# Optimization experiments

Measured on AMD Instinct MI355X. Metric: run time of the kernel, lower is better.

## Reference

```python
import jax, jax.numpy as jnp
import numpy as np

N_EMBD = 384
N_HEAD = 6
HEAD_SIZE = N_EMBD // N_HEAD  # 64
B, T, S = 128, 256, 256
EPS = 1e-5


def setup_inputs() -> dict:
    key = jax.random.key(0)
    ks = jax.random.split(key, 20)
    w = lambda k, shape: (jax.random.normal(k, shape, dtype=jnp.float32) * 0.02)
    inp = {
        'x': jax.random.normal(ks[0], (B, T, N_EMBD), dtype=jnp.float32),
        'encoder_output': jax.random.normal(ks[1], (B, S, N_EMBD), dtype=jnp.float32),
        # masked self-attention heads (stacked over heads): [H, C, D]
        'wq1': w(ks[2], (N_HEAD, N_EMBD, HEAD_SIZE)),
        'wk1': w(ks[3], (N_HEAD, N_EMBD, HEAD_SIZE)),
        'wv1': w(ks[4], (N_HEAD, N_EMBD, HEAD_SIZE)),
        'proj1_w': w(ks[5], (N_EMBD, N_EMBD)),
        'proj1_b': jnp.zeros((N_EMBD,), jnp.float32),
        # cross-attention heads
        'wq2': w(ks[6], (N_HEAD, N_EMBD, HEAD_SIZE)),
        'wk2': w(ks[7], (N_HEAD, N_EMBD, HEAD_SIZE)),
        'wv2': w(ks[8], (N_HEAD, N_EMBD, HEAD_SIZE)),
        'proj2_w': w(ks[9], (N_EMBD, N_EMBD)),
        'proj2_b': jnp.zeros((N_EMBD,), jnp.float32),
        # feed-forward
        'ffn_w1': w(ks[10], (N_EMBD, 4 * N_EMBD)),
        'ffn_b1': jnp.zeros((4 * N_EMBD,), jnp.float32),
        'ffn_w2': w(ks[11], (4 * N_EMBD, N_EMBD)),
        'ffn_b2': jnp.zeros((N_EMBD,), jnp.float32),
        # layernorms
        'ln1_g': jnp.ones((N_EMBD,), jnp.float32), 'ln1_b': jnp.zeros((N_EMBD,), jnp.float32),
        'ln2_g': jnp.ones((N_EMBD,), jnp.float32), 'ln2_b': jnp.zeros((N_EMBD,), jnp.float32),
        'ln3_g': jnp.ones((N_EMBD,), jnp.float32), 'ln3_b': jnp.zeros((N_EMBD,), jnp.float32),
    }
    return inp


def _layernorm(x, g, b):
    mu = jnp.mean(x, axis=-1, keepdims=True)
    var = jnp.mean(jnp.square(x - mu), axis=-1, keepdims=True)
    return (x - mu) * jax.lax.rsqrt(var + EPS) * g + b


def _mha(xq, xkv, wq, wk, wv, proj_w, proj_b, causal):
    # NOTE: source scales by C**-0.5 with C = n_embd (not head_size)
    scale = jnp.asarray(N_EMBD, xq.dtype) ** -0.5
    q = jnp.einsum('btc,hcd->bhtd', xq, wq)
    k = jnp.einsum('bsc,hcd->bhsd', xkv, wk)
    v = jnp.einsum('bsc,hcd->bhsd', xkv, wv)
    wei = jnp.einsum('bhtd,bhsd->bhts', q, k) * scale
    if causal:
        Tq, Tk = xq.shape[1], xkv.shape[1]
        mask = jnp.tril(jnp.ones((Tq, Tk), dtype=bool))
        wei = jnp.where(mask, wei, jnp.asarray(-jnp.inf, wei.dtype))
    p = jax.nn.softmax(wei, axis=-1)  # dropout omitted (eval mode)
    o = jnp.einsum('bhts,bhsd->bhtd', p, v)
    Bq, H, Tq, D = o.shape
    o = o.transpose(0, 2, 1, 3).reshape(Bq, Tq, H * D)  # concat heads
    return o @ proj_w + proj_b


def reference(x, encoder_output,
              wq1, wk1, wv1, proj1_w, proj1_b,
              wq2, wk2, wv2, proj2_w, proj2_b,
              ffn_w1, ffn_b1, ffn_w2, ffn_b2,
              ln1_g, ln1_b, ln2_g, ln2_b, ln3_g, ln3_b):
    # x = x + masked self-attn(ln1(x))
    x = x + _mha(_layernorm(x, ln1_g, ln1_b), _layernorm(x, ln1_g, ln1_b),
                 wq1, wk1, wv1, proj1_w, proj1_b, causal=True)
    # x = x + cross-attn(ln2(x), encoder_output)  (no mask)
    x = x + _mha(_layernorm(x, ln2_g, ln2_b), encoder_output,
                 wq2, wk2, wv2, proj2_w, proj2_b, causal=False)
    # x = x + ffwd(ln3(x))
    h = _layernorm(x, ln3_g, ln3_b)
    x = x + (jax.nn.relu(h @ ffn_w1 + ffn_b1) @ ffn_w2 + ffn_b2)
    return x
```

## Files before the change

### kernel.cpp

```cpp
#include <hip/hip_runtime.h>
#include <hip/hip_bf16.h>

#define BB 128
#define TT 256
#define CC 384
#define HH 6
#define DD 64
#define NTOK 32768

typedef __attribute__((ext_vector_type(8))) short short8;
typedef __attribute__((ext_vector_type(4))) float f32x4;

__device__ __forceinline__ unsigned short f2bf(float f) {
  union { float f; unsigned int u; } v; v.f = f;
  unsigned int r = v.u + 0x7fff + ((v.u >> 16) & 1);
  return (unsigned short)(r >> 16);
}

__device__ __forceinline__ void glds16(const void* g, void* l) {
  __builtin_amdgcn_global_load_lds((const __attribute__((address_space(1))) void*)g,
                                   (__attribute__((address_space(3))) void*)l, 16, 0, 0);
}

__device__ __forceinline__ void vm_drain() {
  asm volatile("s_waitcnt vmcnt(0)" ::: "memory");
  __builtin_amdgcn_sched_barrier(0);
}

__global__ __launch_bounds__(256) void pack_t_k(
    const float* __restrict__ wq1, const float* __restrict__ wk1, const float* __restrict__ wv1,
    const float* __restrict__ wq2, const float* __restrict__ wk2, const float* __restrict__ wv2,
    const float* __restrict__ proj1_w, const float* __restrict__ proj2_w,
    const float* __restrict__ ffn_w1, const float* __restrict__ ffn_w2,
    unsigned short* __restrict__ W) {
  __shared__ unsigned short tile[64 * 72];
  const int id = blockIdx.x;
  const int tid = threadIdx.x;
  const float* src;
  unsigned short* dst;
  int ldIn, ldOut, i0, j0;
  if (id < 216) {
    int w = id / 36, rem = id - w * 36;
    int h = rem / 6, tr = rem - h * 6;
    const float* bases[6] = {wq1, wk1, wv1, wq2, wk2, wv2};
    const int dstOff[6] = {0, 147456, 294912, 442368, 589824, 737280};
    src = bases[w] + h * 24576;
    dst = W + dstOff[w] + h * 24576;
    ldIn = 64; ldOut = 384; i0 = tr * 64; j0 = 0;
  } else if (id < 288) {
    int t = id - 216;
    int which = t / 36; t -= which * 36;
    int tr = t / 6, tc = t - tr * 6;
    src = which ? proj2_w : proj1_w;
    dst = W + (which ? 1032192 : 884736);
    ldIn = 384; ldOut = 384; i0 = tr * 64; j0 = tc * 64;
  } else if (id < 432) {
    int t = id - 288;
    int tr = t / 24, tc = t - tr * 24;
    src = ffn_w1; dst = W + 1179648;
    ldIn = 1536; ldOut = 384; i0 = tr * 64; j0 = tc * 64;
  } else {
    int t = id - 432;
    int tr = t / 6, tc = t - tr * 6;
    src = ffn_w2; dst = W + 1769472;
    ldIn = 384; ldOut = 1536; i0 = tr * 64; j0 = tc * 64;
  }
#pragma unroll
  for (int p = 0; p < 4; ++p) {
    int chunk = p * 256 + tid;
    int r = chunk >> 4, c4 = chunk & 15;
    float4 f = *(const float4*)&src[(size_t)(i0 + r) * ldIn + j0 + c4 * 4];
    tile[(c4 * 4 + 0) * 72 + r] = f2bf(f.x);
    tile[(c4 * 4 + 1) * 72 + r] = f2bf(f.y);
    tile[(c4 * 4 + 2) * 72 + r] = f2bf(f.z);
    tile[(c4 * 4 + 3) * 72 + r] = f2bf(f.w);
  }
  __syncthreads();
#pragma unroll
  for (int p = 0; p < 2; ++p) {
    int chunk = p * 256 + tid;
    int j = chunk >> 3, i8 = chunk & 7;
    *(uint4*)&dst[(size_t)(j0 + j) * ldOut + i0 + i8 * 8] = *(const uint4*)&tile[j * 72 + i8 * 8];
  }
}

__global__ __launch_bounds__(256) void ln_k(const float* __restrict__ x,
                                            unsigned short* __restrict__ out,
                                            const float* __restrict__ gamma,
                                            const float* __restrict__ beta) {
  int row = blockIdx.x * 4 + (threadIdx.x >> 6);
  int lane = threadIdx.x & 63;
  const float2* xr = (const float2*)(x + (size_t)row * CC);
  float2 v[3];
  float s = 0.f;
#pragma unroll
  for (int j = 0; j < 3; ++j) { v[j] = xr[j * 64 + lane]; s += v[j].x + v[j].y; }
#pragma unroll
  for (int m = 1; m < 64; m <<= 1) s += __shfl_xor(s, m);
  float mu = s * (1.0f / CC);
  float vs = 0.f;
#pragma unroll
  for (int j = 0; j < 3; ++j) {
    float dx = v[j].x - mu, dy = v[j].y - mu;
    vs += dx * dx + dy * dy;
  }
#pragma unroll
  for (int m = 1; m < 64; m <<= 1) vs += __shfl_xor(vs, m);
  float rs = rsqrtf(vs * (1.0f / CC) + 1e-5f);
  unsigned int* orow = (unsigned int*)(out + (size_t)row * CC);
#pragma unroll
  for (int j = 0; j < 3; ++j) {
    int cidx = j * 64 + lane;
    float2 gmm = ((const float2*)gamma)[cidx];
    float2 bt = ((const float2*)beta)[cidx];
    unsigned int lo = f2bf((v[j].x - mu) * rs * gmm.x + bt.x);
    unsigned int hi = f2bf((v[j].y - mu) * rs * gmm.y + bt.y);
    orow[cidx] = lo | (hi << 16);
  }
}

template <int EPI, bool AF32, int BM>
__global__ __launch_bounds__(256) void gemm_k(const void* __restrict__ Ap, int lda,
                                              const unsigned short* __restrict__ Bt, int ldb,
                                              void* __restrict__ Cp, int ldc,
                                              const float* __restrict__ bias,
                                              const float* __restrict__ res, int ldres,
                                              int K, int nx) {
  constexpr int MI = BM / 32;
  constexpr int APASS = BM * 8 / 256;
  constexpr int SMEMN = (EPI == 2) ? (BM * 256) : (BM * 64 + 8192);
  __shared__ unsigned short smem[SMEMN];
  unsigned short* sA = smem;
  unsigned short* sB = smem + BM * 64;
  const int tid = threadIdx.x;
  const int chunkg = gridDim.x >> 3;
  const int wg = blockIdx.x;
  const int lg = (wg & 7) * chunkg + (wg >> 3);
  const int bx = lg % nx, by = lg / nx;
  const int m0 = by * BM;
  const int n0 = bx * 128;
  const int wid = tid >> 6, lane = tid & 63;
  const int wr = wid >> 1, wc = wid & 1;
  const int g = lane >> 4, c = lane & 15;

  f32x4 acc[MI][4] = {};
  float biasr[4];
  if (EPI >= 1) {
#pragma unroll
    for (int ni = 0; ni < 4; ++ni) biasr[ni] = bias[n0 + wc * 64 + ni * 16 + c];
  }

  const int nt = K >> 6;
  for (int t = 0; t < nt; ++t) {
    const int k0 = t * 64;
    if constexpr (!AF32) {
#pragma unroll
      for (int p = 0; p < APASS; ++p) {
        int chunk = p * 256 + tid;
        int row = chunk >> 3, grp = chunk & 7;
        const unsigned short* Ab = (const unsigned short*)Ap;
        glds16(&Ab[(size_t)(m0 + row) * lda + k0 + ((grp ^ (row & 7)) << 3)], &sA[chunk * 8]);
      }
    } else {
#pragma unroll
      for (int p = 0; p < APASS; ++p) {
        int chunk = p * 256 + tid;
        int row = chunk >> 3, grp = chunk & 7;
        int dst = row * 64 + ((grp ^ (row & 7)) << 3);
        const float* Af = (const float*)Ap + (size_t)(m0 + row) * lda + k0 + grp * 8;
        float4 f0 = *(const float4*)Af;
        float4 f1 = *(const float4*)(Af + 4);
        union { unsigned short h[8]; uint4 u; } t2;
        t2.h[0] = f2bf(f0.x); t2.h[1] = f2bf(f0.y); t2.h[2] = f2bf(f0.z); t2.h[3] = f2bf(f0.w);
        t2.h[4] = f2bf(f1.x); t2.h[5] = f2bf(f1.y); t2.h[6] = f2bf(f1.z); t2.h[7] = f2bf(f1.w);
        *(uint4*)&sA[dst] = t2.u;
      }
    }
#pragma unroll
    for (int p = 0; p < 4; ++p) {
      int chunk = p * 256 + tid;
      int row = chunk >> 3, grp = chunk & 7;
      glds16(&Bt[(size_t)(n0 + row) * ldb + k0 + ((grp ^ (row & 7)) << 3)], &sB[chunk * 8]);
    }
    vm_drain();
    __syncthreads();
#pragma unroll
    for (int kk = 0; kk < 2; ++kk) {
      short8 a[MI], b[4];
#pragma unroll
      for (int mi = 0; mi < MI; ++mi) {
        int r = wr * (BM / 2) + mi * 16 + c;
        a[mi] = *(const short8*)&sA[r * 64 + (((kk * 4 + g) ^ (r & 7)) << 3)];
      }
#pragma unroll
      for (int ni = 0; ni < 4; ++ni) {
        int rb = wc * 64 + ni * 16 + c;
        b[ni] = *(const short8*)&sB[rb * 64 + (((kk * 4 + g) ^ (rb & 7)) << 3)];
      }
#pragma unroll
      for (int mi = 0; mi < MI; ++mi)
#pragma unroll
        for (int ni = 0; ni < 4; ++ni)
          acc[mi][ni] = __builtin_amdgcn_mfma_f32_16x16x32_bf16(a[mi], b[ni], acc[mi][ni], 0, 0, 0);
    }
    __syncthreads();
  }

  if (EPI <= 1) {
#pragma unroll
    for (int mi = 0; mi < MI; ++mi)
#pragma unroll
      for (int ni = 0; ni < 4; ++ni)
#pragma unroll
        for (int i = 0; i < 4; ++i) {
          int row = wr * (BM / 2) + mi * 16 + g * 4 + i;
          int col = wc * 64 + ni * 16 + c;
          float v = acc[mi][ni][i];
          if (EPI == 1) v = fmaxf(v + biasr[ni], 0.f);
          int gsw = (col >> 3) ^ ((row >> 2) & 7);
          smem[row * 128 + gsw * 8 + (col & 7)] = f2bf(v);
        }
    __syncthreads();
#pragma unroll
    for (int it = 0; it < BM / 16; ++it) {
      int chunk = it * 256 + tid;
      int row = chunk >> 4, c16 = chunk & 15;
      int gsw = c16 ^ ((row >> 2) & 7);
      *(uint4*)&((unsigned short*)Cp)[(size_t)(m0 + row) * ldc + n0 + c16 * 8] =
          *(const uint4*)&smem[row * 128 + gsw * 8];
    }
  } else {
    float* smf = (float*)smem;
#pragma unroll
    for (int mi = 0; mi < MI; ++mi)
#pragma unroll
      for (int ni = 0; ni < 4; ++ni)
#pragma unroll
        for (int i = 0; i < 4; ++i) {
          int row = wr * (BM / 2) + mi * 16 + g * 4 + i;
          int col = wc * 64 + ni * 16 + c;
          int gg = col >> 2;
          int sg = gg ^ (row & 7);
          smf[row * 128 + sg * 4 + (col & 3)] = acc[mi][ni][i] + biasr[ni];
        }
    __syncthreads();
#pragma unroll
    for (int it = 0; it < BM / 8; ++it) {
      int chunk = it * 256 + tid;
      int row = chunk >> 5, gg = chunk & 31;
      int sg = gg ^ (row & 7);
      float4 v = *(const float4*)&smf[row * 128 + sg * 4];
      float4 r = *(const float4*)&res[(size_t)(m0 + row) * ldres + n0 + gg * 4];
      float4 o;
      o.x = v.x + r.x; o.y = v.y + r.y; o.z = v.z + r.z; o.w = v.w + r.w;
      *(float4*)&((float*)Cp)[(size_t)(m0 + row) * ldc + n0 + gg * 4] = o;
    }
  }
}

__global__ __launch_bounds__(512, 2) void gemm_ln_k(
    const unsigned short* __restrict__ Ab, const unsigned short* __restrict__ Bt,
    const float* __restrict__ bias, const float* __restrict__ res,
    float* __restrict__ xc, const float* __restrict__ gamma,
    const float* __restrict__ beta, unsigned short* __restrict__ xn) {
  __shared__ unsigned short smem[28672];
  __shared__ float part[64][8];
  unsigned short* sA = smem;
  unsigned short* sB = smem + 4096;
  const int tid = threadIdx.x;
  const int chunkg = gridDim.x >> 3;
  const int wg = blockIdx.x;
  const int lg = (wg & 7) * chunkg + (wg >> 3);
  const int m0 = lg * 64;
  const int wid = tid >> 6, lane = tid & 63;
  const int wr = wid >> 2, wcg = wid & 3;
  const int g = lane >> 4, c = lane & 15;

  f32x4 acc[2][6] = {};
  float biasr[6], gam[6], bet[6];
#pragma unroll
  for (int ni = 0; ni < 6; ++ni) {
    int col = wcg * 96 + ni * 16 + c;
    biasr[ni] = bias[col]; gam[ni] = gamma[col]; bet[ni] = beta[col];
  }

  for (int t = 0; t < 6; ++t) {
    const int k0 = t * 64;
    {
      int chunk = tid;
      int row = chunk >> 3, grp = chunk & 7;
      glds16(&Ab[(size_t)(m0 + row) * 384 + k0 + ((grp ^ (row & 7)) << 3)], &sA[chunk * 8]);
    }
#pragma unroll
    for (int p = 0; p < 6; ++p) {
      int chunk = p * 512 + tid;
      int row = chunk >> 3, grp = chunk & 7;
      glds16(&Bt[(size_t)row * 384 + k0 + ((grp ^ (row & 7)) << 3)], &sB[chunk * 8]);
    }
    vm_drain();
    __syncthreads();
#pragma unroll
    for (int kk = 0; kk < 2; ++kk) {
      short8 a[2], b[6];
#pragma unroll
      for (int mi = 0; mi < 2; ++mi) {
        int r = wr * 32 + mi * 16 + c;
        a[mi] = *(const short8*)&sA[r * 64 + (((kk * 4 + g) ^ (r & 7)) << 3)];
      }
#pragma unroll
      for (int ni = 0; ni < 6; ++ni) {
        int rb = wcg * 96 + ni * 16 + c;
        b[ni] = *(const short8*)&sB[rb * 64 + (((kk * 4 + g) ^ (rb & 7)) << 3)];
      }
#pragma unroll
      for (int mi = 0; mi < 2; ++mi)
#pragma unroll
        for (int ni = 0; ni < 6; ++ni)
          acc[mi][ni] = __builtin_amdgcn_mfma_f32_16x16x32_bf16(a[mi], b[ni], acc[mi][ni], 0, 0, 0);
    }
    __syncthreads();
  }

#pragma unroll
  for (int mi = 0; mi < 2; ++mi)
#pragma unroll
    for (int i = 0; i < 4; ++i) {
      int row = m0 + wr * 32 + mi * 16 + g * 4 + i;
#pragma unroll
      for (int ni = 0; ni < 6; ++ni)
        acc[mi][ni][i] += biasr[ni] + res[(size_t)row * 384 + wcg * 96 + ni * 16 + c];
    }

#pragma unroll
  for (int mi = 0; mi < 2; ++mi)
#pragma unroll
    for (int i = 0; i < 4; ++i) {
      float s = 0.f, q = 0.f;
#pragma unroll
      for (int ni = 0; ni < 6; ++ni) { float v = acc[mi][ni][i]; s += v; q += v * v; }
#pragma unroll
      for (int m = 1; m < 16; m <<= 1) { s += __shfl_xor(s, m); q += __shfl_xor(q, m); }
      if (c == 0) {
        int lr = wr * 32 + mi * 16 + g * 4 + i;
        part[lr][wcg] = s;
        part[lr][4 + wcg] = q;
      }
    }
  __syncthreads();
  float mu[2][4], rs[2][4];
#pragma unroll
  for (int mi = 0; mi < 2; ++mi)
#pragma unroll
    for (int i = 0; i < 4; ++i) {
      int lr = wr * 32 + mi * 16 + g * 4 + i;
      float s = part[lr][0] + part[lr][1] + part[lr][2] + part[lr][3];
      float q = part[lr][4] + part[lr][5] + part[lr][6] + part[lr][7];
      float m_ = s * (1.0f / 384.f);
      mu[mi][i] = m_;
      rs[mi][i] = rsqrtf(q * (1.0f / 384.f) - m_ * m_ + 1e-5f);
    }

  float* bf = (float*)smem;
#pragma unroll
  for (int h = 0; h < 2; ++h) {
    __syncthreads();
    if (wr == h) {
#pragma unroll
      for (int mi = 0; mi < 2; ++mi)
#pragma unroll
        for (int ni = 0; ni < 6; ++ni)
#pragma unroll
          for (int i = 0; i < 4; ++i) {
            int lr = mi * 16 + g * 4 + i;
            bf[lr * 388 + wcg * 96 + ni * 16 + c] = acc[mi][ni][i];
          }
    }
    __syncthreads();
#pragma unroll
    for (int p = 0; p < 6; ++p) {
      int chunk = p * 512 + tid;
      int row = chunk / 96, gg = chunk % 96;
      float4 v = *(const float4*)&bf[row * 388 + gg * 4];
      *(float4*)&xc[(size_t)(m0 + h * 32 + row) * 384 + gg * 4] = v;
    }
  }

  __syncthreads();
#pragma unroll
  for (int mi = 0; mi < 2; ++mi)
#pragma unroll
    for (int ni = 0; ni < 6; ++ni)
#pragma unroll
      for (int i = 0; i < 4; ++i) {
        int lr = wr * 32 + mi * 16 + g * 4 + i;
        smem[lr * 392 + wcg * 96 + ni * 16 + c] =
            f2bf((acc[mi][ni][i] - mu[mi][i]) * rs[mi][i] * gam[ni] + bet[ni]);
      }
  __syncthreads();
#pragma unroll
  for (int p = 0; p < 6; ++p) {
    int chunk = p * 512 + tid;
    int row = chunk / 48, c8 = chunk % 48;
    *(uint4*)&xn[(size_t)(m0 + row) * 384 + c8 * 8] = *(const uint4*)&smem[row * 392 + c8 * 8];
  }
}

__device__ __forceinline__ int vt_off(int d, int sgrp) {
  return d * 256 + ((((sgrp + (d >> 3)) & 31) ^ (d & 7)) << 3);
}

template <bool CAUSAL>
__global__ __launch_bounds__(512, 2) void attn_k(const unsigned short* __restrict__ QKV,
                                                 unsigned short* __restrict__ O) {
  __shared__ unsigned short Ks[256 * 64];
  __shared__ unsigned short Vt[64 * 256];
  __shared__ unsigned short Ps[8][16 * 40];
  const int bh = blockIdx.x >> 1;
  const int half = blockIdx.x & 1;
  const int b = bh / HH, hh = bh - b * HH;
  const int tid = threadIdx.x, wid = tid >> 6, lane = tid & 63;
  const int g = lane >> 4, c = lane & 15;
  const unsigned short* base = QKV + (size_t)b * TT * 1152;

#pragma unroll
  for (int t = 0; t < 4; ++t) {
    int chunk = t * 512 + tid;
    int s = chunk >> 3, grp = chunk & 7;
    *(uint4*)&Ks[s * 64 + ((grp ^ (s & 7)) << 3)] =
        *(const uint4*)&base[(size_t)s * 1152 + 384 + hh * 64 + grp * 8];
    union { unsigned short h[8]; uint4 u; } tv;
    tv.u = *(const uint4*)&base[(size_t)s * 1152 + 768 + hh * 64 + grp * 8];
#pragma unroll
    for (int j = 0; j < 8; ++j) Vt[vt_off(grp * 8 + j, s >> 3) + (s & 7)] = tv.h[j];
  }
  __syncthreads();

  const float scale = 0.05103103630798287f;
  unsigned short* Pw = &Ps[wid][0];
  const int qr0 = half * 128 + wid * 16;

  short8 aq[2];
#pragma unroll
  for (int kk = 0; kk < 2; ++kk)
    aq[kk] = *(const short8*)&QKV[(size_t)(b * TT + qr0 + c) * 1152 + hh * 64 + kk * 32 + g * 8];

  f32x4 sacc[16] = {};
#pragma unroll
  for (int sj = 0; sj < 16; ++sj) {
    if (!CAUSAL || sj * 16 <= qr0) {
      int rk = sj * 16 + c;
      f32x4 z = sacc[sj];
      z = __builtin_amdgcn_mfma_f32_16x16x32_bf16(
          aq[0], *(const short8*)&Ks[rk * 64 + ((g ^ (rk & 7)) << 3)], z, 0, 0, 0);
      z = __builtin_amdgcn_mfma_f32_16x16x32_bf16(
          aq[1], *(const short8*)&Ks[rk * 64 + (((4 + g) ^ (rk & 7)) << 3)], z, 0, 0, 0);
      sacc[sj] = z;
    }
  }

  float inv[4];
#pragma unroll
  for (int i = 0; i < 4; ++i) {
    const int qr = qr0 + g * 4 + i;
    float mx = -1e30f;
#pragma unroll
    for (int sj = 0; sj < 16; ++sj) {
      if (!CAUSAL || sj * 16 <= qr0) {
        int s = sj * 16 + c;
        float v = sacc[sj][i] * scale;
        if (CAUSAL && s > qr) v = -1e30f;
        sacc[sj][i] = v;
        mx = fmaxf(mx, v);
      }
    }
#pragma unroll
    for (int m = 1; m < 16; m <<= 1) mx = fmaxf(mx, __shfl_xor(mx, m));
    float sum = 0.f;
#pragma unroll
    for (int sj = 0; sj < 16; ++sj) {
      if (!CAUSAL || sj * 16 <= qr0) {
        float p = __expf(sacc[sj][i] - mx);
        sacc[sj][i] = p;
        sum += p;
      }
    }
#pragma unroll
    for (int m = 1; m < 16; m <<= 1) sum += __shfl_xor(sum, m);
    inv[i] = 1.0f / sum;
  }

  f32x4 oacc[4] = {};
#pragma unroll
  for (int sk = 0; sk < 8; ++sk) {
    if (!CAUSAL || sk * 32 <= qr0) {
#pragma unroll
      for (int half_sj = 0; half_sj < 2; ++half_sj) {
        int sj = sk * 2 + half_sj;
#pragma unroll
        for (int i = 0; i < 4; ++i)
          Pw[(g * 4 + i) * 40 + half_sj * 16 + c] = f2bf(sacc[sj][i]);
      }
      short8 ap = *(const short8*)&Pw[c * 40 + g * 8];
#pragma unroll
      for (int dj = 0; dj < 4; ++dj) {
        short8 bv = *(const short8*)&Vt[vt_off(dj * 16 + c, sk * 4 + g)];
        oacc[dj] = __builtin_amdgcn_mfma_f32_16x16x32_bf16(ap, bv, oacc[dj], 0, 0, 0);
      }
    }
  }

  __syncthreads();
#pragma unroll
  for (int dj = 0; dj < 4; ++dj)
#pragma unroll
    for (int i = 0; i < 4; ++i) {
      int lr = wid * 16 + g * 4 + i;
      int col = dj * 16 + c;
      int gsw = (col >> 3) ^ ((lr >> 2) & 7);
      Ks[lr * 64 + gsw * 8 + (col & 7)] = f2bf(oacc[dj][i] * inv[i]);
    }
  __syncthreads();
#pragma unroll
  for (int it = 0; it < 2; ++it) {
    int chunk = it * 512 + tid;
    int row = chunk >> 3, c8 = chunk & 7;
    int gsw = c8 ^ ((row >> 2) & 7);
    *(uint4*)&O[(size_t)(b * TT + half * 128 + row) * CC + hh * 64 + c8 * 8] =
        *(const uint4*)&Ks[row * 64 + gsw * 8];
  }
}

extern "C" void kernel_launch(void* const* d_in, const int* in_sizes, int n_in,
                              void* d_out, int out_size, void* d_ws, size_t ws_size,
                              hipStream_t stream) {
  const float* x = (const float*)d_in[0];
  const float* enc = (const float*)d_in[1];
  const float* wq1 = (const float*)d_in[2];
  const float* wk1 = (const float*)d_in[3];
  const float* wv1 = (const float*)d_in[4];
  const float* proj1_w = (const float*)d_in[5];
  const float* proj1_b = (const float*)d_in[6];
  const float* wq2 = (const float*)d_in[7];
  const float* wk2 = (const float*)d_in[8];
  const float* wv2 = (const float*)d_in[9];
  const float* proj2_w = (const float*)d_in[10];
  const float* proj2_b = (const float*)d_in[11];
  const float* ffn_w1 = (const float*)d_in[12];
  const float* ffn_b1 = (const float*)d_in[13];
  const float* ffn_w2 = (const float*)d_in[14];
  const float* ffn_b2 = (const float*)d_in[15];
  const float* ln1_g = (const float*)d_in[16];
  const float* ln1_b = (const float*)d_in[17];
  const float* ln2_g = (const float*)d_in[18];
  const float* ln2_b = (const float*)d_in[19];
  const float* ln3_g = (const float*)d_in[20];
  const float* ln3_b = (const float*)d_in[21];
  float* out = (float*)d_out;

  char* ws = (char*)d_ws;
  const size_t OFF_A = 0;
  const size_t OFF_X = 50331648;
  const size_t OFF_Q = 75497472;
  const size_t OFF_O = 150994944;
  const size_t OFF_W = 176160768;

  float* xc = (float*)(ws + OFF_A);
  unsigned short* xn = (unsigned short*)(ws + OFF_X);
  unsigned short* qkv = (unsigned short*)(ws + OFF_Q);
  unsigned short* h1 = (unsigned short*)(ws + OFF_Q);
  unsigned short* obuf = (unsigned short*)(ws + OFF_O);
  unsigned short* W = (unsigned short*)(ws + OFF_W);

  unsigned short* Wqkv1t = W + 0;
  unsigned short* Wq2t = W + 442368;
  unsigned short* Wkv2t = W + 589824;
  unsigned short* proj1t = W + 884736;
  unsigned short* proj2t = W + 1032192;
  unsigned short* W1t = W + 1179648;
  unsigned short* W2t = W + 1769472;

  pack_t_k<<<576, 256, 0, stream>>>(wq1, wk1, wv1, wq2, wk2, wv2,
                                    proj1_w, proj2_w, ffn_w1, ffn_w2, W);

  dim3 blk(256);
  ln_k<<<8192, blk, 0, stream>>>(x, xn, ln1_g, ln1_b);
  gemm_k<0, false, 128><<<2304, blk, 0, stream>>>(xn, 384, Wqkv1t, 384, qkv, 1152,
                                                  nullptr, nullptr, 0, 384, 9);
  attn_k<true><<<1536, 512, 0, stream>>>(qkv, obuf);
  gemm_ln_k<<<512, 512, 0, stream>>>(obuf, proj1t, proj1_b, x, xc, ln2_g, ln2_b, xn);
  gemm_k<0, false, 128><<<768, blk, 0, stream>>>(xn, 384, Wq2t, 384, qkv, 1152,
                                                 nullptr, nullptr, 0, 384, 3);
  gemm_k<0, true, 128><<<1536, blk, 0, stream>>>(enc, 384, Wkv2t, 384, qkv + 384, 1152,
                                                 nullptr, nullptr, 0, 384, 6);
  attn_k<false><<<1536, 512, 0, stream>>>(qkv, obuf);
  gemm_ln_k<<<512, 512, 0, stream>>>(obuf, proj2t, proj2_b, xc, xc, ln3_g, ln3_b, xn);
  gemm_k<1, false, 128><<<3072, blk, 0, stream>>>(xn, 384, W1t, 384, h1, 1536,
                                                  ffn_b1, nullptr, 0, 384, 12);
  gemm_k<2, false, 64><<<1536, blk, 0, stream>>>(h1, 1536, W2t, 1536, out, 384,
                                                 ffn_b2, xc, 384, 1536, 3);
}
```

Before: 399.2 us.

## Process all query rows per attention block and enlarge FFN2 GEMM tile

Each attention block now covers all 256 query rows of a batch-head instead of half. Every warp handles two 16-row query blocks, so K and V are staged into LDS once per head rather than twice, and the grid halves. The FFN2 GEMM moves from 64-row to 128-row tiles. Its fp32 residual epilogue is staged through shared memory in two 64-row halves so the LDS footprint stays fixed. The trade-off is fewer blocks, which means more wave-quantization tail and, in the causal case, more uneven work across warps.

```diff
diff --git a/kernel.cpp b/kernel.cpp
--- a/kernel.cpp
+++ b/kernel.cpp
@@ -128,7 +128,7 @@
                                               int K, int nx) {
   constexpr int MI = BM / 32;
   constexpr int APASS = BM * 8 / 256;
-  constexpr int SMEMN = (EPI == 2) ? (BM * 256) : (BM * 64 + 8192);
+  constexpr int SMEMN = BM * 64 + 8192;
   __shared__ unsigned short smem[SMEMN];
   unsigned short* sA = smem;
   unsigned short* sB = smem + BM * 64;
@@ -230,30 +230,38 @@
           *(const uint4*)&smem[row * 128 + gsw * 8];
     }
   } else {
+    constexpr int NH = BM / 64;
     float* smf = (float*)smem;
 #pragma unroll
-    for (int mi = 0; mi < MI; ++mi)
-#pragma unroll
-      for (int ni = 0; ni < 4; ++ni)
-#pragma unroll
-        for (int i = 0; i < 4; ++i) {
-          int row = wr * (BM / 2) + mi * 16 + g * 4 + i;
-          int col = wc * 64 + ni * 16 + c;
-          int gg = col >> 2;
-          int sg = gg ^ (row & 7);
-          smf[row * 128 + sg * 4 + (col & 3)] = acc[mi][ni][i] + biasr[ni];
-        }
-    __syncthreads();
-#pragma unroll
-    for (int it = 0; it < BM / 8; ++it) {
-      int chunk = it * 256 + tid;
-      int row = chunk >> 5, gg = chunk & 31;
-      int sg = gg ^ (row & 7);
-      float4 v = *(const float4*)&smf[row * 128 + sg * 4];
-      float4 r = *(const float4*)&res[(size_t)(m0 + row) * ldres + n0 + gg * 4];
-      float4 o;
-      o.x = v.x + r.x; o.y = v.y + r.y; o.z = v.z + r.z; o.w = v.w + r.w;
-      *(float4*)&((float*)Cp)[(size_t)(m0 + row) * ldc + n0 + gg * 4] = o;
+    for (int hh = 0; hh < NH; ++hh) {
+      if (hh) __syncthreads();
+      if (NH == 1 || wr == hh) {
+#pragma unroll
+        for (int mi = 0; mi < MI; ++mi)
+#pragma unroll
+          for (int ni = 0; ni < 4; ++ni)
+#pragma unroll
+            for (int i = 0; i < 4; ++i) {
+              int row = (NH == 1 ? wr * 32 : 0) + mi * 16 + g * 4 + i;
+              int col = wc * 64 + ni * 16 + c;
+              int gg = col >> 2;
+              int sg = gg ^ (row & 7);
+              smf[row * 128 + sg * 4 + (col & 3)] = acc[mi][ni][i] + biasr[ni];
+            }
+      }
+      __syncthreads();
+#pragma unroll
+      for (int it = 0; it < 8; ++it) {
+        int chunk = it * 256 + tid;
+        int row = chunk >> 5, gg = chunk & 31;
+        int sg = gg ^ (row & 7);
+        float4 v = *(const float4*)&smf[row * 128 + sg * 4];
+        int grow = m0 + hh * 64 + row;
+        float4 r = *(const float4*)&res[(size_t)grow * ldres + n0 + gg * 4];
+        float4 o;
+        o.x = v.x + r.x; o.y = v.y + r.y; o.z = v.z + r.z; o.w = v.w + r.w;
+        *(float4*)&((float*)Cp)[(size_t)grow * ldc + n0 + gg * 4] = o;
+      }
     }
   }
 }
@@ -415,8 +423,7 @@
   __shared__ unsigned short Ks[256 * 64];
   __shared__ unsigned short Vt[64 * 256];
   __shared__ unsigned short Ps[8][16 * 40];
-  const int bh = blockIdx.x >> 1;
-  const int half = blockIdx.x & 1;
+  const int bh = blockIdx.x;
   const int b = bh / HH, hh = bh - b * HH;
   const int tid = threadIdx.x, wid = tid >> 6, lane = tid & 63;
   const int g = lane >> 4, c = lane & 15;
@@ -437,95 +444,100 @@
 
   const float scale = 0.05103103630798287f;
   unsigned short* Pw = &Ps[wid][0];
-  const int qr0 = half * 128 + wid * 16;
-
-  short8 aq[2];
-#pragma unroll
-  for (int kk = 0; kk < 2; ++kk)
-    aq[kk] = *(const short8*)&QKV[(size_t)(b * TT + qr0 + c) * 1152 + hh * 64 + kk * 32 + g * 8];
-
-  f32x4 sacc[16] = {};
-#pragma unroll
-  for (int sj = 0; sj < 16; ++sj) {
-    if (!CAUSAL || sj * 16 <= qr0) {
-      int rk = sj * 16 + c;
-      f32x4 z = sacc[sj];
-      z = __builtin_amdgcn_mfma_f32_16x16x32_bf16(
-          aq[0], *(const short8*)&Ks[rk * 64 + ((g ^ (rk & 7)) << 3)], z, 0, 0, 0);
-      z = __builtin_amdgcn_mfma_f32_16x16x32_bf16(
-          aq[1], *(const short8*)&Ks[rk * 64 + (((4 + g) ^ (rk & 7)) << 3)], z, 0, 0, 0);
-      sacc[sj] = z;
-    }
-  }
-
-  float inv[4];
-#pragma unroll
-  for (int i = 0; i < 4; ++i) {
-    const int qr = qr0 + g * 4 + i;
-    float mx = -1e30f;
+
+  f32x4 oacc[2][4] = {};
+  float inv[2][4];
+#pragma unroll
+  for (int qb = 0; qb < 2; ++qb) {
+    const int qr0 = wid * 32 + qb * 16;
+    short8 aq[2];
+#pragma unroll
+    for (int kk = 0; kk < 2; ++kk)
+      aq[kk] = *(const short8*)&QKV[(size_t)(b * TT + qr0 + c) * 1152 + hh * 64 + kk * 32 + g * 8];
+
+    f32x4 sacc[16] = {};
 #pragma unroll
     for (int sj = 0; sj < 16; ++sj) {
       if (!CAUSAL || sj * 16 <= qr0) {
-        int s = sj * 16 + c;
-        float v = sacc[sj][i] * scale;
-        if (CAUSAL && s > qr) v = -1e30f;
-        sacc[sj][i] = v;
-        mx = fmaxf(mx, v);
-      }
-    }
-#pragma unroll
-    for (int m = 1; m < 16; m <<= 1) mx = fmaxf(mx, __shfl_xor(mx, m));
-    float sum = 0.f;
-#pragma unroll
-    for (int sj = 0; sj < 16; ++sj) {
-      if (!CAUSAL || sj * 16 <= qr0) {
-        float p = __expf(sacc[sj][i] - mx);
-        sacc[sj][i] = p;
-        sum += p;
-      }
-    }
-#pragma unroll
-    for (int m = 1; m < 16; m <<= 1) sum += __shfl_xor(sum, m);
-    inv[i] = 1.0f / sum;
-  }
-
-  f32x4 oacc[4] = {};
-#pragma unroll
-  for (int sk = 0; sk < 8; ++sk) {
-    if (!CAUSAL || sk * 32 <= qr0) {
-#pragma unroll
-      for (int half_sj = 0; half_sj < 2; ++half_sj) {
-        int sj = sk * 2 + half_sj;
-#pragma unroll
-        for (int i = 0; i < 4; ++i)
-          Pw[(g * 4 + i) * 40 + half_sj * 16 + c] = f2bf(sacc[sj][i]);
-      }
-      short8 ap = *(const short8*)&Pw[c * 40 + g * 8];
-#pragma unroll
-      for (int dj = 0; dj < 4; ++dj) {
-        short8 bv = *(const short8*)&Vt[vt_off(dj * 16 + c, sk * 4 + g)];
-        oacc[dj] = __builtin_amdgcn_mfma_f32_16x16x32_bf16(ap, bv, oacc[dj], 0, 0, 0);
+        int rk = sj * 16 + c;
+        f32x4 z = sacc[sj];
+        z = __builtin_amdgcn_mfma_f32_16x16x32_bf16(
+            aq[0], *(const short8*)&Ks[rk * 64 + ((g ^ (rk & 7)) << 3)], z, 0, 0, 0);
+        z = __builtin_amdgcn_mfma_f32_16x16x32_bf16(
+            aq[1], *(const short8*)&Ks[rk * 64 + (((4 + g) ^ (rk & 7)) << 3)], z, 0, 0, 0);
+        sacc[sj] = z;
+      }
+    }
+
+#pragma unroll
+    for (int i = 0; i < 4; ++i) {
+      const int qr = qr0 + g * 4 + i;
+      float mx = -1e30f;
+#pragma unroll
+      for (int sj = 0; sj < 16; ++sj) {
+        if (!CAUSAL || sj * 16 <= qr0) {
+          int s = sj * 16 + c;
+          float v = sacc[sj][i] * scale;
+          if (CAUSAL && s > qr) v = -1e30f;
+          sacc[sj][i] = v;
+          mx = fmaxf(mx, v);
+        }
+      }
+#pragma unroll
+      for (int m = 1; m < 16; m <<= 1) mx = fmaxf(mx, __shfl_xor(mx, m));
+      float sum = 0.f;
+#pragma unroll
+      for (int sj = 0; sj < 16; ++sj) {
+        if (!CAUSAL || sj * 16 <= qr0) {
+          float p = __expf(sacc[sj][i] - mx);
+          sacc[sj][i] = p;
+          sum += p;
+        }
+      }
+#pragma unroll
+      for (int m = 1; m < 16; m <<= 1) sum += __shfl_xor(sum, m);
+      inv[qb][i] = 1.0f / sum;
+    }
+
+#pragma unroll
+    for (int sk = 0; sk < 8; ++sk) {
+      if (!CAUSAL || sk * 32 <= qr0) {
+#pragma unroll
+        for (int half_sj = 0; half_sj < 2; ++half_sj) {
+          int sj = sk * 2 + half_sj;
+#pragma unroll
+          for (int i = 0; i < 4; ++i)
+            Pw[(g * 4 + i) * 40 + half_sj * 16 + c] = f2bf(sacc[sj][i]);
+        }
+        short8 ap = *(const short8*)&Pw[c * 40 + g * 8];
+#pragma unroll
+        for (int dj = 0; dj < 4; ++dj) {
+          short8 bv = *(const short8*)&Vt[vt_off(dj * 16 + c, sk * 4 + g)];
+          oacc[qb][dj] = __builtin_amdgcn_mfma_f32_16x16x32_bf16(ap, bv, oacc[qb][dj], 0, 0, 0);
+        }
       }
     }
   }
 
   __syncthreads();
 #pragma unroll
-  for (int dj = 0; dj < 4; ++dj)
-#pragma unroll
-    for (int i = 0; i < 4; ++i) {
-      int lr = wid * 16 + g * 4 + i;
-      int col = dj * 16 + c;
-      int gsw = (col >> 3) ^ ((lr >> 2) & 7);
-      Ks[lr * 64 + gsw * 8 + (col & 7)] = f2bf(oacc[dj][i] * inv[i]);
-    }
+  for (int qb = 0; qb < 2; ++qb)
+#pragma unroll
+    for (int dj = 0; dj < 4; ++dj)
+#pragma unroll
+      for (int i = 0; i < 4; ++i) {
+        int lr = wid * 32 + qb * 16 + g * 4 + i;
+        int col = dj * 16 + c;
+        int gsw = (col >> 3) ^ ((lr >> 2) & 7);
+        Ks[lr * 64 + gsw * 8 + (col & 7)] = f2bf(oacc[qb][dj][i] * inv[qb][i]);
+      }
   __syncthreads();
 #pragma unroll
-  for (int it = 0; it < 2; ++it) {
+  for (int it = 0; it < 4; ++it) {
     int chunk = it * 512 + tid;
     int row = chunk >> 3, c8 = chunk & 7;
     int gsw = c8 ^ ((row >> 2) & 7);
-    *(uint4*)&O[(size_t)(b * TT + half * 128 + row) * CC + hh * 64 + c8 * 8] =
+    *(uint4*)&O[(size_t)(b * TT + row) * CC + hh * 64 + c8 * 8] =
         *(const uint4*)&Ks[row * 64 + gsw * 8];
   }
 }
@@ -586,16 +598,16 @@
   ln_k<<<8192, blk, 0, stream>>>(x, xn, ln1_g, ln1_b);
   gemm_k<0, false, 128><<<2304, blk, 0, stream>>>(xn, 384, Wqkv1t, 384, qkv, 1152,
                                                   nullptr, nullptr, 0, 384, 9);
-  attn_k<true><<<1536, 512, 0, stream>>>(qkv, obuf);
+  attn_k<true><<<768, 512, 0, stream>>>(qkv, obuf);
   gemm_ln_k<<<512, 512, 0, stream>>>(obuf, proj1t, proj1_b, x, xc, ln2_g, ln2_b, xn);
   gemm_k<0, false, 128><<<768, blk, 0, stream>>>(xn, 384, Wq2t, 384, qkv, 1152,
                                                  nullptr, nullptr, 0, 384, 3);
   gemm_k<0, true, 128><<<1536, blk, 0, stream>>>(enc, 384, Wkv2t, 384, qkv + 384, 1152,
                                                  nullptr, nullptr, 0, 384, 6);
-  attn_k<false><<<1536, 512, 0, stream>>>(qkv, obuf);
+  attn_k<false><<<768, 512, 0, stream>>>(qkv, obuf);
   gemm_ln_k<<<512, 512, 0, stream>>>(obuf, proj2t, proj2_b, xc, xc, ln3_g, ln3_b, xn);
   gemm_k<1, false, 128><<<3072, blk, 0, stream>>>(xn, 384, W1t, 384, h1, 1536,
                                                   ffn_b1, nullptr, 0, 384, 12);
-  gemm_k<2, false, 64><<<1536, blk, 0, stream>>>(h1, 1536, W2t, 1536, out, 384,
+  gemm_k<2, false, 128><<<768, blk, 0, stream>>>(h1, 1536, W2t, 1536, out, 384,
                                                  ffn_b2, xc, 384, 1536, 3);
 }
```

New measurement: 429.4 us. +7.6%, slower.

## Add dedicated FFN2 kernel computing full 384-wide rows per block

Applied to the files above, without the earlier changes.

Replaces the generic FFN down-projection GEMM (64x128 tiles, 1536 blocks) with a specialized kernel where each block computes a 32-row by full-384-column output tile. A is loaded once per row tile instead of three times, and the residual add and bias are fused into the epilogue. Each wave now holds 2x6 accumulators, and the kernel loads the full B slice (384x64) per k-step without double buffering. The epilogue path for EPI==2 is removed from the generic kernel.

```diff
diff --git a/kernel.cpp b/kernel.cpp
--- a/kernel.cpp
+++ b/kernel.cpp
@@ -124,12 +124,10 @@
                                               const unsigned short* __restrict__ Bt, int ldb,
                                               void* __restrict__ Cp, int ldc,
                                               const float* __restrict__ bias,
-                                              const float* __restrict__ res, int ldres,
                                               int K, int nx) {
   constexpr int MI = BM / 32;
   constexpr int APASS = BM * 8 / 256;
-  constexpr int SMEMN = (EPI == 2) ? (BM * 256) : (BM * 64 + 8192);
-  __shared__ unsigned short smem[SMEMN];
+  __shared__ unsigned short smem[BM * 64 + 8192];
   unsigned short* sA = smem;
   unsigned short* sB = smem + BM * 64;
   const int tid = threadIdx.x;
@@ -206,55 +204,110 @@
     __syncthreads();
   }
 
-  if (EPI <= 1) {
-#pragma unroll
-    for (int mi = 0; mi < MI; ++mi)
-#pragma unroll
-      for (int ni = 0; ni < 4; ++ni)
-#pragma unroll
-        for (int i = 0; i < 4; ++i) {
-          int row = wr * (BM / 2) + mi * 16 + g * 4 + i;
-          int col = wc * 64 + ni * 16 + c;
-          float v = acc[mi][ni][i];
-          if (EPI == 1) v = fmaxf(v + biasr[ni], 0.f);
-          int gsw = (col >> 3) ^ ((row >> 2) & 7);
-          smem[row * 128 + gsw * 8 + (col & 7)] = f2bf(v);
-        }
-    __syncthreads();
-#pragma unroll
-    for (int it = 0; it < BM / 16; ++it) {
-      int chunk = it * 256 + tid;
-      int row = chunk >> 4, c16 = chunk & 15;
-      int gsw = c16 ^ ((row >> 2) & 7);
-      *(uint4*)&((unsigned short*)Cp)[(size_t)(m0 + row) * ldc + n0 + c16 * 8] =
-          *(const uint4*)&smem[row * 128 + gsw * 8];
-    }
-  } else {
-    float* smf = (float*)smem;
-#pragma unroll
-    for (int mi = 0; mi < MI; ++mi)
-#pragma unroll
-      for (int ni = 0; ni < 4; ++ni)
-#pragma unroll
-        for (int i = 0; i < 4; ++i) {
-          int row = wr * (BM / 2) + mi * 16 + g * 4 + i;
-          int col = wc * 64 + ni * 16 + c;
-          int gg = col >> 2;
-          int sg = gg ^ (row & 7);
-          smf[row * 128 + sg * 4 + (col & 3)] = acc[mi][ni][i] + biasr[ni];
-        }
-    __syncthreads();
-#pragma unroll
-    for (int it = 0; it < BM / 8; ++it) {
-      int chunk = it * 256 + tid;
-      int row = chunk >> 5, gg = chunk & 31;
-      int sg = gg ^ (row & 7);
-      float4 v = *(const float4*)&smf[row * 128 + sg * 4];
-      float4 r = *(const float4*)&res[(size_t)(m0 + row) * ldres + n0 + gg * 4];
-      float4 o;
-      o.x = v.x + r.x; o.y = v.y + r.y; o.z = v.z + r.z; o.w = v.w + r.w;
-      *(float4*)&((float*)Cp)[(size_t)(m0 + row) * ldc + n0 + gg * 4] = o;
-    }
+#pragma unroll
+  for (int mi = 0; mi < MI; ++mi)
+#pragma unroll
+    for (int ni = 0; ni < 4; ++ni)
+#pragma unroll
+      for (int i = 0; i < 4; ++i) {
+        int row = wr * (BM / 2) + mi * 16 + g * 4 + i;
+        int col = wc * 64 + ni * 16 + c;
+        float v = acc[mi][ni][i];
+        if (EPI == 1) v = fmaxf(v + biasr[ni], 0.f);
+        int gsw = (col >> 3) ^ ((row >> 2) & 7);
+        smem[row * 128 + gsw * 8 + (col & 7)] = f2bf(v);
+      }
+  __syncthreads();
+#pragma unroll
+  for (int it = 0; it < BM / 16; ++it) {
+    int chunk = it * 256 + tid;
+    int row = chunk >> 4, c16 = chunk & 15;
+    int gsw = c16 ^ ((row >> 2) & 7);
+    *(uint4*)&((unsigned short*)Cp)[(size_t)(m0 + row) * ldc + n0 + c16 * 8] =
+        *(const uint4*)&smem[row * 128 + gsw * 8];
+  }
+}
+
+__global__ __launch_bounds__(256) void ffn2_k(const unsigned short* __restrict__ h1,
+                                              const unsigned short* __restrict__ W2t,
+                                              float* __restrict__ out,
+                                              const float* __restrict__ b2,
+                                              const float* __restrict__ res) {
+  __shared__ unsigned short smem[26624];
+  unsigned short* sA = smem;
+  unsigned short* sB = smem + 2048;
+  const int tid = threadIdx.x;
+  const int wg = blockIdx.x;
+  const int lg = (wg & 7) * (gridDim.x >> 3) + (wg >> 3);
+  const int m0 = lg * 32;
+  const int w = tid >> 6, lane = tid & 63;
+  const int g = lane >> 4, c = lane & 15;
+
+  f32x4 acc[2][6] = {};
+  float biasr[6];
+#pragma unroll
+  for (int ni = 0; ni < 6; ++ni) biasr[ni] = b2[w * 96 + ni * 16 + c];
+
+  for (int t = 0; t < 24; ++t) {
+    const int k0 = t * 64;
+    {
+      int row = tid >> 3, grp = tid & 7;
+      glds16(&h1[(size_t)(m0 + row) * 1536 + k0 + ((grp ^ (row & 7)) << 3)], &sA[tid * 8]);
+    }
+#pragma unroll
+    for (int p = 0; p < 12; ++p) {
+      int chunk = p * 256 + tid;
+      int row = chunk >> 3, grp = chunk & 7;
+      glds16(&W2t[(size_t)row * 1536 + k0 + ((grp ^ (row & 7)) << 3)], &sB[chunk * 8]);
+    }
+    vm_drain();
+    __syncthreads();
+#pragma unroll
+    for (int kk = 0; kk < 2; ++kk) {
+      short8 a[2], b[6];
+#pragma unroll
+      for (int mi = 0; mi < 2; ++mi) {
+        int r = mi * 16 + c;
+        a[mi] = *(const short8*)&sA[r * 64 + (((kk * 4 + g) ^ (r & 7)) << 3)];
+      }
+#pragma unroll
+      for (int ni = 0; ni < 6; ++ni) {
+        int rb = w * 96 + ni * 16 + c;
+        b[ni] = *(const short8*)&sB[rb * 64 + (((kk * 4 + g) ^ (rb & 7)) << 3)];
+      }
+#pragma unroll
+      for (int mi = 0; mi < 2; ++mi)
+#pragma unroll
+        for (int ni = 0; ni < 6; ++ni)
+          acc[mi][ni] = __builtin_amdgcn_mfma_f32_16x16x32_bf16(a[mi], b[ni], acc[mi][ni], 0, 0, 0);
+    }
+    __syncthreads();
+  }
+
+  float* smf = (float*)smem;
+#pragma unroll
+  for (int mi = 0; mi < 2; ++mi)
+#pragma unroll
+    for (int ni = 0; ni < 6; ++ni)
+#pragma unroll
+      for (int i = 0; i < 4; ++i) {
+        int row = mi * 16 + g * 4 + i;
+        int col = w * 96 + ni * 16 + c;
+        int gg = col >> 2;
+        int sg = (gg & ~7) | ((gg ^ row) & 7);
+        smf[row * 388 + sg * 4 + (col & 3)] = acc[mi][ni][i] + biasr[ni];
+      }
+  __syncthreads();
+#pragma unroll
+  for (int it = 0; it < 12; ++it) {
+    int chunk = it * 256 + tid;
+    int row = chunk / 96, gg = chunk % 96;
+    int sg = (gg & ~7) | ((gg ^ row) & 7);
+    float4 v = *(const float4*)&smf[row * 388 + sg * 4];
+    float4 r = *(const float4*)&res[(size_t)(m0 + row) * 384 + gg * 4];
+    float4 o;
+    o.x = v.x + r.x; o.y = v.y + r.y; o.z = v.z + r.z; o.w = v.w + r.w;
+    *(float4*)&out[(size_t)(m0 + row) * 384 + gg * 4] = o;
   }
 }
 
@@ -585,17 +638,16 @@
   dim3 blk(256);
   ln_k<<<8192, blk, 0, stream>>>(x, xn, ln1_g, ln1_b);
   gemm_k<0, false, 128><<<2304, blk, 0, stream>>>(xn, 384, Wqkv1t, 384, qkv, 1152,
-                                                  nullptr, nullptr, 0, 384, 9);
+                                                  nullptr, 384, 9);
   attn_k<true><<<1536, 512, 0, stream>>>(qkv, obuf);
   gemm_ln_k<<<512, 512, 0, stream>>>(obuf, proj1t, proj1_b, x, xc, ln2_g, ln2_b, xn);
   gemm_k<0, false, 128><<<768, blk, 0, stream>>>(xn, 384, Wq2t, 384, qkv, 1152,
-                                                 nullptr, nullptr, 0, 384, 3);
+                                                 nullptr, 384, 3);
   gemm_k<0, true, 128><<<1536, blk, 0, stream>>>(enc, 384, Wkv2t, 384, qkv + 384, 1152,
-                                                 nullptr, nullptr, 0, 384, 6);
+                                                 nullptr, 384, 6);
   attn_k<false><<<1536, 512, 0, stream>>>(qkv, obuf);
   gemm_ln_k<<<512, 512, 0, stream>>>(obuf, proj2t, proj2_b, xc, xc, ln3_g, ln3_b, xn);
   gemm_k<1, false, 128><<<3072, blk, 0, stream>>>(xn, 384, W1t, 384, h1, 1536,
-                                                  ffn_b1, nullptr, 0, 384, 12);
-  gemm_k<2, false, 64><<<1536, blk, 0, stream>>>(h1, 1536, W2t, 1536, out, 384,
-                                                 ffn_b2, xc, 384, 1536, 3);
-}
+                                                  ffn_b1, 384, 12);
+  ffn2_k<<<1024, blk, 0, stream>>>(h1, W2t, out, ffn_b2, xc);
+}
```

Measured after the change: 429.1 us. 1.07x slower.
